# Kernel tuning notes

Measured on AMD Instinct MI355X. Metric: run time of the kernel, lower is better.

## Reference

```python
import jax, jax.numpy as jnp
import numpy as np

B, N, KNN, C, H, LK, CEMB, GDIM = 16, 512, 20, 256, 128, 4, 64, 64


def _lrelu(x, slope):
    return jnp.where(x >= 0, x, slope * x)


def _forward(img_feat, graph_feat, roi_mask_bit, prev_x_id, prev_y_id, knn_idx,
             conv_w, conv_b, pre_w1, pre_b1, pre_w2, pre_b2,
             g1_w, g1_gamma, g1_beta, g1_mean, g1_var,
             g2_w, g2_gamma, g2_beta, g2_mean, g2_var,
             q_w1, q_b1, q_w2, q_b2, q_w3, q_b3):
    lk = conv_w.shape[-1]
    bsz = img_feat.shape[0]
    # Index2Feat: conv with padding = lk-1 -> (B, CEMB, H+lk-1, W+lk-1)
    patches = jax.lax.conv_general_dilated(img_feat, conv_w, (1, 1), [(lk - 1, lk - 1)] * 2)
    patches = patches + conv_b[None, :, None, None]
    p = jnp.transpose(patches, (0, 2, 3, 1))  # (B, Hp, Wp, CEMB)
    bi = jnp.arange(bsz)[:, None]
    yy, xx = 2 * prev_y_id, 2 * prev_x_id
    sf1 = p[bi, yy, xx]
    sf2 = p[bi, yy + lk, xx]
    sf3 = p[bi, yy, xx + lk]
    sf4 = p[bi, yy + lk, xx + lk]
    local = jnp.concatenate([sf1, sf2, sf3, sf4], axis=-1)  # (B, N, 4*CEMB)
    local = local * jnp.transpose(roi_mask_bit, (0, 2, 1))  # detached mask
    local = jnp.concatenate([local, jnp.transpose(graph_feat, (0, 2, 1))], axis=-1)  # (B,N,320)
    # pre_graph MLP (LeakyReLU 0.01, doLastAct=True)
    h = _lrelu(local @ pre_w1 + pre_b1, 0.01)
    h = _lrelu(h @ pre_w2 + pre_b2, 0.01)  # (B, N, C)
    knn = knn_idx[0]  # (N, K) shared across batch

    def edgeconv(x, w, gamma, beta, mean, var):
        xk = x[:, knn]  # (B, N, K, C) neighbor gather
        xc = jnp.broadcast_to(x[:, :, None, :], xk.shape)
        e = jnp.concatenate([xk - xc, xc], axis=-1)  # (B, N, K, 2C)
        y = jnp.einsum('bnkc,oc->bnko', e, w)  # 1x1 conv, no bias
        y = (y - mean) * (gamma / jnp.sqrt(var + 1e-5)) + beta  # BN (inference)
        return _lrelu(y, 0.2).max(axis=2)  # max over k neighbors

    h = edgeconv(h, g1_w, g1_gamma, g1_beta, g1_mean, g1_var)
    h = edgeconv(h, g2_w, g2_gamma, g2_beta, g2_mean, g2_var)
    # query MLP (256 -> 256 -> 64 -> 2), LeakyReLU 0.01, no last act
    q = _lrelu(h @ q_w1 + q_b1, 0.01)
    q = _lrelu(q @ q_w2 + q_b2, 0.01)
    bits = q @ q_w3 + q_b3  # (B, N, 2)
    return jnp.transpose(bits, (0, 2, 1)), jnp.transpose(h, (0, 2, 1))


def setup_inputs() -> dict:
    key = jax.random.key(0)
    ks = jax.random.split(key, 24)
    s = 0.02
    img_feat = jax.random.normal(ks[0], (B, C, H, H), jnp.float32)
    graph_feat = jax.random.normal(ks[1], (B, GDIM, N), jnp.float32)
    roi_mask_bit = jnp.ones((B, 1, N), jnp.float32)
    prev_x_id = jax.random.randint(ks[2], (B, N), 0, H // 2, jnp.int32)
    prev_y_id = jax.random.randint(ks[3], (B, N), 0, H // 2, jnp.int32)
    # knn graph from normalized 3D keypoints (computed once at init in torch)
    p3d = jax.random.uniform(ks[4], (1, 3, N), jnp.float32, -1.0, 1.0)
    inner = -2.0 * jnp.einsum('bdn,bdm->bnm', p3d, p3d)
    xsq = jnp.sum(p3d ** 2, axis=1, keepdims=True)  # (1,1,N)
    pd = -xsq - inner - jnp.transpose(xsq, (0, 2, 1))
    knn_idx = jax.lax.top_k(pd, KNN)[1].astype(jnp.int32)  # (1, N, KNN)
    return {
        'img_feat': img_feat, 'graph_feat': graph_feat, 'roi_mask_bit': roi_mask_bit,
        'prev_x_id': prev_x_id, 'prev_y_id': prev_y_id, 'knn_idx': knn_idx,
        'conv_w': jax.random.normal(ks[5], (CEMB, C, LK, LK), jnp.float32) * s,
        'conv_b': jnp.zeros((CEMB,), jnp.float32),
        'pre_w1': jax.random.normal(ks[6], (4 * CEMB + GDIM, C), jnp.float32) * s,
        'pre_b1': jnp.zeros((C,), jnp.float32),
        'pre_w2': jax.random.normal(ks[7], (C, C), jnp.float32) * s,
        'pre_b2': jnp.zeros((C,), jnp.float32),
        'g1_w': jax.random.normal(ks[8], (C, 2 * C), jnp.float32) * s,
        'g1_gamma': jnp.ones((C,), jnp.float32), 'g1_beta': jnp.zeros((C,), jnp.float32),
        'g1_mean': jnp.zeros((C,), jnp.float32), 'g1_var': jnp.ones((C,), jnp.float32),
        'g2_w': jax.random.normal(ks[9], (C, 2 * C), jnp.float32) * s,
        'g2_gamma': jnp.ones((C,), jnp.float32), 'g2_beta': jnp.zeros((C,), jnp.float32),
        'g2_mean': jnp.zeros((C,), jnp.float32), 'g2_var': jnp.ones((C,), jnp.float32),
        'q_w1': jax.random.normal(ks[10], (C, C), jnp.float32) * s,
        'q_b1': jnp.zeros((C,), jnp.float32),
        'q_w2': jax.random.normal(ks[11], (C, 64), jnp.float32) * s,
        'q_b2': jnp.zeros((64,), jnp.float32),
        'q_w3': jax.random.normal(ks[12], (64, 2), jnp.float32) * s,
        'q_b3': jnp.zeros((2,), jnp.float32),
    }


def reference(img_feat, graph_feat, roi_mask_bit, prev_x_id, prev_y_id, knn_idx,
              conv_w, conv_b, pre_w1, pre_b1, pre_w2, pre_b2,
              g1_w, g1_gamma, g1_beta, g1_mean, g1_var,
              g2_w, g2_gamma, g2_beta, g2_mean, g2_var,
              q_w1, q_b1, q_w2, q_b2, q_w3, q_b3):
    return _forward(img_feat, graph_feat, roi_mask_bit, prev_x_id, prev_y_id, knn_idx,
                    conv_w, conv_b, pre_w1, pre_b1, pre_w2, pre_b2,
                    g1_w, g1_gamma, g1_beta, g1_mean, g1_var,
                    g2_w, g2_gamma, g2_beta, g2_mean, g2_var,
                    q_w1, q_b1, q_w2, q_b2, q_w3, q_b3)
```

## Files before the change

kernel.cpp:

```cpp
#include <hip/hip_runtime.h>


typedef __bf16 bf16_t;
typedef bf16_t bf16x8 __attribute__((ext_vector_type(8)));
typedef float  f32x4  __attribute__((ext_vector_type(4)));

static constexpr int BATCH = 16;
static constexpr int NPT   = 512;
static constexpr int PTS   = BATCH * NPT;
static constexpr int CONVM = PTS * 4;
static constexpr int CONVK = 4096;

static constexpr size_t OFF_WCONV_OLD = 0;
static constexpr size_t OFF_WCONVP    = OFF_WCONV_OLD + (size_t)64*4096*2;
static constexpr size_t OFF_WPRE1     = OFF_WCONVP    + (size_t)64*4096*2;
static constexpr size_t OFF_WPRE2     = OFF_WPRE1     + (size_t)256*320*2;
static constexpr size_t OFF_WEC1      = OFF_WPRE2     + (size_t)256*256*2;
static constexpr size_t OFF_WEC2      = OFF_WEC1      + (size_t)512*256*2;
static constexpr size_t OFF_WQ1       = OFF_WEC2      + (size_t)512*256*2;
static constexpr size_t OFF_WQ2       = OFF_WQ1       + (size_t)256*256*2;
static constexpr size_t OFF_LOCAL     = OFF_WQ2       + (size_t)64*256*2;
static constexpr size_t OFF_X         = OFF_LOCAL + (size_t)PTS*320*2;
static constexpr size_t OFF_Y         = OFF_X     + (size_t)PTS*256*2;
static constexpr size_t OFF_Z         = OFF_Y     + (size_t)PTS*256*2;
static constexpr size_t OFF_UNION     = OFF_Z     + (size_t)PTS*64*2;
static constexpr size_t AB_BYTES      = (size_t)PTS*512*4;
static constexpr size_t IMGT_BYTES    = (size_t)16*128*128*256*2;
static constexpr size_t WS_BASE       = OFF_UNION + AB_BYTES;
static constexpr size_t WS_FULL       = OFF_UNION + IMGT_BYTES;

static constexpr int WP_CONV  = 64*4096;
static constexpr int WP_CONVP = 64*4096;
static constexpr int WP_PRE1 = 256*320;
static constexpr int WP_PRE2 = 256*256;
static constexpr int WP_EC   = 512*256;
static constexpr int WP_Q1   = 256*256;
static constexpr int WP_Q2   = 64*256;
static constexpr int WP_TOTAL = WP_CONV + WP_CONVP + WP_PRE1 + WP_PRE2 + 2*WP_EC + WP_Q1 + WP_Q2;

__global__ __launch_bounds__(256) void wprep_kernel(
    const float* __restrict__ conv_w, const float* __restrict__ pre_w1,
    const float* __restrict__ pre_w2, const float* __restrict__ g1_w,
    const float* __restrict__ g2_w,   const float* __restrict__ q_w1,
    const float* __restrict__ q_w2,
    bf16_t* __restrict__ wt_conv, bf16_t* __restrict__ wt_convp,
    bf16_t* __restrict__ wt_pre1,
    bf16_t* __restrict__ wt_pre2, bf16_t* __restrict__ wt_ec1,
    bf16_t* __restrict__ wt_ec2,  bf16_t* __restrict__ wt_q1,
    bf16_t* __restrict__ wt_q2)
{
    int i = blockIdx.x * 256 + threadIdx.x;
    if (i >= WP_TOTAL) return;
    if (i < WP_CONV) { wt_conv[i] = (bf16_t)conv_w[i]; return; }
    i -= WP_CONV;
    if (i < WP_CONVP) {
        const int o = i >> 12, pix = (i >> 8) & 15, c = i & 255;
        wt_convp[i] = (bf16_t)conv_w[((o * 256 + c) << 4) + pix]; return; }
    i -= WP_CONVP;
    if (i < WP_PRE1) { int n = i / 320, k = i - n * 320;
        wt_pre1[i] = (bf16_t)pre_w1[k * 256 + n]; return; }
    i -= WP_PRE1;
    if (i < WP_PRE2) { int n = i >> 8, k = i & 255;
        wt_pre2[i] = (bf16_t)pre_w2[k * 256 + n]; return; }
    i -= WP_PRE2;
    if (i < WP_EC) { int n = i >> 8, k = i & 255;
        wt_ec1[i] = (bf16_t)(n < 256 ? g1_w[n * 512 + k] : g1_w[(n - 256) * 512 + 256 + k]);
        return; }
    i -= WP_EC;
    if (i < WP_EC) { int n = i >> 8, k = i & 255;
        wt_ec2[i] = (bf16_t)(n < 256 ? g2_w[n * 512 + k] : g2_w[(n - 256) * 512 + 256 + k]);
        return; }
    i -= WP_EC;
    if (i < WP_Q1) { int n = i >> 8, k = i & 255;
        wt_q1[i] = (bf16_t)q_w1[k * 256 + n]; return; }
    i -= WP_Q1;
    { int n = i >> 8, k = i & 255;
        wt_q2[i] = (bf16_t)q_w2[k * 64 + n]; }
}

__global__ __launch_bounds__(256) void transpose_img(
    const float* __restrict__ img, bf16_t* __restrict__ imgT)
{
    __shared__ float T[64][65];
    const int bid = blockIdx.x;
    const int cc = bid & 3;
    const int xh = (bid >> 2) & 1;
    const int y  = (bid >> 3) & 127;
    const int b  = bid >> 10;
    const int t = threadIdx.x;
    const int x0 = xh * 64, c0 = cc * 64;
    {
        const int px = t & 63, cr = t >> 6;
        const float* src = img + ((size_t)(b * 256 + c0 + cr) * 128 + y) * 128 + x0 + px;
        #pragma unroll
        for (int i = 0; i < 16; ++i)
            T[cr + i * 4][px] = src[(size_t)i * 4 * 16384];
    }
    __syncthreads();
    {
        const int cl = t & 63, pr = t >> 6;
        bf16_t* dst = imgT + ((size_t)(b * 128 + y) * 128 + x0) * 256 + c0 + cl;
        #pragma unroll
        for (int i = 0; i < 16; ++i) {
            const int pxl = pr + i * 4;
            dst[(size_t)pxl * 256] = (bf16_t)T[cl][pxl];
        }
    }
}

__global__ __launch_bounds__(256) void conv_gather_gemm2(
    const bf16_t* __restrict__ imgT,
    const bf16_t* __restrict__ Wc,
    const float* __restrict__ conv_b, const float* __restrict__ roi,
    const int* __restrict__ px, const int* __restrict__ py,
    bf16_t* __restrict__ local)
{
    __shared__ bf16_t As[64][136];
    __shared__ bf16_t Bs[64][136];
    const int tid = threadIdx.x, lane = tid & 63, wave = tid >> 6;
    const int wm = wave & 1, wn = wave >> 1;
    const int row0 = blockIdx.x * 64;
    const int sm = tid >> 2, sq = tid & 3;
    const int r = row0 + sm, corner = r & 3, pnt = r >> 2, b = pnt >> 9;
    const int oy = 2 * py[pnt] + (corner & 1) * 4;
    const int ox = 2 * px[pnt] + ((corner >> 1) & 1) * 4;
    const bf16_t* imgb = imgT + (size_t)b * (128 * 128 * 256);
    const int e0 = sq * 8;

    f32x4 acc[2][2] = {};
    #pragma unroll 1
    for (int s = 0; s < 32; ++s) {
        const int pix = s >> 1, h = s & 1;
        const int iy = oy - 3 + (pix >> 2), ix = ox - 3 + (pix & 3);
        if (((unsigned)iy < 128u) && ((unsigned)ix < 128u)) {
            const bf16_t* srcA = imgb + ((size_t)(iy * 128 + ix)) * 256 + h * 128 + e0;
            #pragma unroll
            for (int i = 0; i < 4; ++i)
                *(uint4*)&As[sm][e0 + i * 32] = *(const uint4*)(srcA + i * 32);
        } else {
            const uint4 z = {0, 0, 0, 0};
            #pragma unroll
            for (int i = 0; i < 4; ++i)
                *(uint4*)&As[sm][e0 + i * 32] = z;
        }
        {
            const bf16_t* srcB = Wc + (size_t)sm * 4096 + pix * 256 + h * 128 + e0;
            #pragma unroll
            for (int i = 0; i < 4; ++i)
                *(uint4*)&Bs[sm][e0 + i * 32] = *(const uint4*)(srcB + i * 32);
        }
        __syncthreads();
        #pragma unroll
        for (int kk = 0; kk < 128; kk += 32) {
            const int kf = kk + ((lane >> 4) << 3);
            bf16x8 a0 = *(const bf16x8*)&As[wm * 32 + (lane & 15)][kf];
            bf16x8 a1 = *(const bf16x8*)&As[wm * 32 + 16 + (lane & 15)][kf];
            bf16x8 b0 = *(const bf16x8*)&Bs[wn * 32 + (lane & 15)][kf];
            bf16x8 b1 = *(const bf16x8*)&Bs[wn * 32 + 16 + (lane & 15)][kf];
            acc[0][0] = __builtin_amdgcn_mfma_f32_16x16x32_bf16(a0, b0, acc[0][0], 0, 0, 0);
            acc[0][1] = __builtin_amdgcn_mfma_f32_16x16x32_bf16(a0, b1, acc[0][1], 0, 0, 0);
            acc[1][0] = __builtin_amdgcn_mfma_f32_16x16x32_bf16(a1, b0, acc[1][0], 0, 0, 0);
            acc[1][1] = __builtin_amdgcn_mfma_f32_16x16x32_bf16(a1, b1, acc[1][1], 0, 0, 0);
        }
        __syncthreads();
    }
    const int crow = (lane >> 4) << 2;
    const int ccol = lane & 15;
    #pragma unroll
    for (int i = 0; i < 2; ++i) {
        #pragma unroll
        for (int j = 0; j < 2; ++j) {
            const int o = wn * 32 + j * 16 + ccol;
            const float bv = conv_b[o];
            #pragma unroll
            for (int rg = 0; rg < 4; ++rg) {
                const int gr = row0 + wm * 32 + i * 16 + crow + rg;
                const int cn = gr & 3;
                const int pp = gr >> 2;
                const float v = (acc[i][j][rg] + bv) * roi[pp];
                local[(size_t)pp * 320 + cn * 64 + o] = (bf16_t)v;
            }
        }
    }
}

__global__ __launch_bounds__(256) void conv_gather_gemm(
    const float* __restrict__ img, const bf16_t* __restrict__ Wc,
    const float* __restrict__ conv_b, const float* __restrict__ roi,
    const int* __restrict__ px, const int* __restrict__ py,
    bf16_t* __restrict__ local)
{
    __shared__ bf16_t As[64][72];
    __shared__ bf16_t Bs[64][72];
    const int tid = threadIdx.x;
    const int lane = tid & 63;
    const int wave = tid >> 6;
    const int wm = wave & 1, wn = wave >> 1;
    const int row0 = blockIdx.x * 64;
    const int sm = tid >> 2;
    const int cq = tid & 3;
    const int r = row0 + sm;
    const int corner = r & 3;
    const int pnt = r >> 2;
    const int b = pnt >> 9;
    const int oy = 2 * py[pnt] + (corner & 1) * 4;
    const int ox = 2 * px[pnt] + ((corner >> 1) & 1) * 4;
    const int iy0 = oy - 3, ix0 = ox - 3;
    const float* imgb = img + (size_t)b * (256 * 128 * 128);

    f32x4 acc[2][2] = {};
    for (int kt = 0; kt < CONVK; kt += 64) {
        {
            const int c = (kt >> 4) + cq;
            const float* ip = imgb + (size_t)c * (128 * 128);
            alignas(16) bf16_t vals[16];
            #pragma unroll
            for (int ky = 0; ky < 4; ++ky) {
                const int iy = iy0 + ky;
                const bool yok = (unsigned)iy < 128u;
                #pragma unroll
                for (int kx = 0; kx < 4; ++kx) {
                    const int ix = ix0 + kx;
                    float v = (yok && (unsigned)ix < 128u) ? ip[iy * 128 + ix] : 0.0f;
                    vals[ky * 4 + kx] = (bf16_t)v;
                }
            }
            *(uint4*)&As[sm][cq * 16]     = *(const uint4*)&vals[0];
            *(uint4*)&As[sm][cq * 16 + 8] = *(const uint4*)&vals[8];
        }
        {
            const bf16_t* src = Wc + (size_t)sm * CONVK + kt + cq * 16;
            *(uint4*)&Bs[sm][cq * 16]     = *(const uint4*)src;
            *(uint4*)&Bs[sm][cq * 16 + 8] = *(const uint4*)(src + 8);
        }
        __syncthreads();
        #pragma unroll
        for (int kk = 0; kk < 64; kk += 32) {
            const int kf = kk + ((lane >> 4) << 3);
            bf16x8 a0 = *(const bf16x8*)&As[wm * 32 + (lane & 15)][kf];
            bf16x8 a1 = *(const bf16x8*)&As[wm * 32 + 16 + (lane & 15)][kf];
            bf16x8 b0 = *(const bf16x8*)&Bs[wn * 32 + (lane & 15)][kf];
            bf16x8 b1 = *(const bf16x8*)&Bs[wn * 32 + 16 + (lane & 15)][kf];
            acc[0][0] = __builtin_amdgcn_mfma_f32_16x16x32_bf16(a0, b0, acc[0][0], 0, 0, 0);
            acc[0][1] = __builtin_amdgcn_mfma_f32_16x16x32_bf16(a0, b1, acc[0][1], 0, 0, 0);
            acc[1][0] = __builtin_amdgcn_mfma_f32_16x16x32_bf16(a1, b0, acc[1][0], 0, 0, 0);
            acc[1][1] = __builtin_amdgcn_mfma_f32_16x16x32_bf16(a1, b1, acc[1][1], 0, 0, 0);
        }
        __syncthreads();
    }
    const int crow = (lane >> 4) << 2;
    const int ccol = lane & 15;
    #pragma unroll
    for (int i = 0; i < 2; ++i) {
        #pragma unroll
        for (int j = 0; j < 2; ++j) {
            const int o = wn * 32 + j * 16 + ccol;
            const float bv = conv_b[o];
            #pragma unroll
            for (int rg = 0; rg < 4; ++rg) {
                const int gr = row0 + wm * 32 + i * 16 + crow + rg;
                const int cn = gr & 3;
                const int pp = gr >> 2;
                const float v = (acc[i][j][rg] + bv) * roi[pp];
                local[(size_t)pp * 320 + cn * 64 + o] = (bf16_t)v;
            }
        }
    }
}

__global__ __launch_bounds__(256) void graph_fill(
    const float* __restrict__ g, bf16_t* __restrict__ local)
{
    const int e = blockIdx.x * 256 + threadIdx.x;
    const int j = e & 63, p = e >> 6;
    const int b = p >> 9, n = p & 511;
    local[(size_t)p * 320 + 256 + j] = (bf16_t)g[((size_t)(b * 64 + j) << 9) + n];
}

template<int K, int N, int ACT>
__global__ __launch_bounds__(256) void gemm_bf16(
    const bf16_t* __restrict__ A, const bf16_t* __restrict__ Bt,
    const float* __restrict__ bias, float slope,
    bf16_t* __restrict__ outB, float* __restrict__ outF)
{
    __shared__ bf16_t As[64][72];
    __shared__ bf16_t Bs[64][72];
    const int tid = threadIdx.x;
    const int lane = tid & 63;
    const int wave = tid >> 6;
    const int wm = wave & 1, wn = wave >> 1;
    const int row0 = blockIdx.x * 64;
    const int col0 = blockIdx.y * 64;
    const int sm = tid >> 2;
    const int sq = (tid & 3) << 4;

    f32x4 acc[2][2] = {};
    for (int kt = 0; kt < K; kt += 64) {
        {
            const bf16_t* src = A + (size_t)(row0 + sm) * K + kt + sq;
            *(uint4*)&As[sm][sq]     = *(const uint4*)src;
            *(uint4*)&As[sm][sq + 8] = *(const uint4*)(src + 8);
        }
        {
            const bf16_t* src = Bt + (size_t)(col0 + sm) * K + kt + sq;
            *(uint4*)&Bs[sm][sq]     = *(const uint4*)src;
            *(uint4*)&Bs[sm][sq + 8] = *(const uint4*)(src + 8);
        }
        __syncthreads();
        #pragma unroll
        for (int kk = 0; kk < 64; kk += 32) {
            const int kf = kk + ((lane >> 4) << 3);
            bf16x8 a0 = *(const bf16x8*)&As[wm * 32 + (lane & 15)][kf];
            bf16x8 a1 = *(const bf16x8*)&As[wm * 32 + 16 + (lane & 15)][kf];
            bf16x8 b0 = *(const bf16x8*)&Bs[wn * 32 + (lane & 15)][kf];
            bf16x8 b1 = *(const bf16x8*)&Bs[wn * 32 + 16 + (lane & 15)][kf];
            acc[0][0] = __builtin_amdgcn_mfma_f32_16x16x32_bf16(a0, b0, acc[0][0], 0, 0, 0);
            acc[0][1] = __builtin_amdgcn_mfma_f32_16x16x32_bf16(a0, b1, acc[0][1], 0, 0, 0);
            acc[1][0] = __builtin_amdgcn_mfma_f32_16x16x32_bf16(a1, b0, acc[1][0], 0, 0, 0);
            acc[1][1] = __builtin_amdgcn_mfma_f32_16x16x32_bf16(a1, b1, acc[1][1], 0, 0, 0);
        }
        __syncthreads();
    }
    const int crow = (lane >> 4) << 2;
    const int ccol = lane & 15;
    #pragma unroll
    for (int i = 0; i < 2; ++i) {
        #pragma unroll
        for (int j = 0; j < 2; ++j) {
            const int gcol = col0 + wn * 32 + j * 16 + ccol;
            const float bv = bias ? bias[gcol] : 0.0f;
            #pragma unroll
            for (int rg = 0; rg < 4; ++rg) {
                const int grow = row0 + wm * 32 + i * 16 + crow + rg;
                float v = acc[i][j][rg] + bv;
                if (ACT == 1) v = v >= 0.0f ? v : slope * v;
                if (outB) outB[(size_t)grow * N + gcol] = (bf16_t)v;
                if (outF) outF[(size_t)grow * N + gcol] = v;
            }
        }
    }
}

__global__ __launch_bounds__(256) void edge_combine(
    const float* __restrict__ AB, const int* __restrict__ knn,
    const float* __restrict__ gamma, const float* __restrict__ beta,
    const float* __restrict__ mean,  const float* __restrict__ var,
    bf16_t* __restrict__ outB, float* __restrict__ outT)
{
    const int p = blockIdx.x;
    const int b = p >> 9, n = p & 511;
    const int o = threadIdx.x;
    const float sc = gamma[o] / sqrtf(var[o] + 1e-5f);
    const float sh = beta[o] - mean[o] * sc;
    const float* rowp = AB + (size_t)p * 512;
    const float d = rowp[256 + o] - rowp[o];
    const float* batch = AB + ((size_t)(b << 9)) * 512;
    float m = -3.4e38f;
    #pragma unroll 4
    for (int k = 0; k < 20; ++k) {
        const int q = knn[n * 20 + k];
        const float v = batch[(size_t)q * 512 + o] + d;
        float y = v * sc + sh;
        y = y >= 0.0f ? y : 0.2f * y;
        m = fmaxf(m, y);
    }
    outB[(size_t)p * 256 + o] = (bf16_t)m;
    if (outT) outT[((size_t)(b * 256 + o) << 9) + n] = m;
}

__global__ __launch_bounds__(256) void q3_kernel(
    const bf16_t* __restrict__ Z, const float* __restrict__ w3,
    const float* __restrict__ b3, float* __restrict__ out)
{
    const int p = blockIdx.x * 256 + threadIdx.x;
    const int b = p >> 9, n = p & 511;
    const bf16_t* q = Z + (size_t)p * 64;
    float s0 = b3[0], s1 = b3[1];
    #pragma unroll
    for (int c = 0; c < 64; ++c) {
        const float v = (float)q[c];
        s0 += v * w3[2 * c];
        s1 += v * w3[2 * c + 1];
    }
    out[(size_t)(b * 2 + 0) * 512 + n] = s0;
    out[(size_t)(b * 2 + 1) * 512 + n] = s1;
}

extern "C" void kernel_launch(void* const* d_in, const int* in_sizes, int n_in,
                              void* d_out, int out_size, void* d_ws, size_t ws_size,
                              hipStream_t stream)
{
    const float* img      = (const float*)d_in[0];
    const float* graph    = (const float*)d_in[1];
    const float* roi      = (const float*)d_in[2];
    const int*   px       = (const int*)d_in[3];
    const int*   py       = (const int*)d_in[4];
    const int*   knn      = (const int*)d_in[5];
    const float* conv_w   = (const float*)d_in[6];
    const float* conv_b   = (const float*)d_in[7];
    const float* pre_w1   = (const float*)d_in[8];
    const float* pre_b1   = (const float*)d_in[9];
    const float* pre_w2   = (const float*)d_in[10];
    const float* pre_b2   = (const float*)d_in[11];
    const float* g1_w     = (const float*)d_in[12];
    const float* g1_gamma = (const float*)d_in[13];
    const float* g1_beta  = (const float*)d_in[14];
    const float* g1_mean  = (const float*)d_in[15];
    const float* g1_var   = (const float*)d_in[16];
    const float* g2_w     = (const float*)d_in[17];
    const float* g2_gamma = (const float*)d_in[18];
    const float* g2_beta  = (const float*)d_in[19];
    const float* g2_mean  = (const float*)d_in[20];
    const float* g2_var   = (const float*)d_in[21];
    const float* q_w1     = (const float*)d_in[22];
    const float* q_b1     = (const float*)d_in[23];
    const float* q_w2     = (const float*)d_in[24];
    const float* q_b2     = (const float*)d_in[25];
    const float* q_w3     = (const float*)d_in[26];
    const float* q_b3     = (const float*)d_in[27];
    float* out = (float*)d_out;

    if (ws_size < WS_BASE) return;

    char* ws = (char*)d_ws;
    bf16_t* wt_conv  = (bf16_t*)(ws + OFF_WCONV_OLD);
    bf16_t* wt_convp = (bf16_t*)(ws + OFF_WCONVP);
    bf16_t* wt_pre1  = (bf16_t*)(ws + OFF_WPRE1);
    bf16_t* wt_pre2  = (bf16_t*)(ws + OFF_WPRE2);
    bf16_t* wt_ec1   = (bf16_t*)(ws + OFF_WEC1);
    bf16_t* wt_ec2   = (bf16_t*)(ws + OFF_WEC2);
    bf16_t* wt_q1    = (bf16_t*)(ws + OFF_WQ1);
    bf16_t* wt_q2    = (bf16_t*)(ws + OFF_WQ2);
    bf16_t* local    = (bf16_t*)(ws + OFF_LOCAL);
    bf16_t* X        = (bf16_t*)(ws + OFF_X);
    bf16_t* Y        = (bf16_t*)(ws + OFF_Y);
    bf16_t* Z        = (bf16_t*)(ws + OFF_Z);
    float*  AB       = (float*)(ws + OFF_UNION);
    bf16_t* imgT     = (bf16_t*)(ws + OFF_UNION);

    const bool big = ws_size >= WS_FULL;

    wprep_kernel<<<(WP_TOTAL + 255) / 256, 256, 0, stream>>>(
        conv_w, pre_w1, pre_w2, g1_w, g2_w, q_w1, q_w2,
        wt_conv, wt_convp, wt_pre1, wt_pre2, wt_ec1, wt_ec2, wt_q1, wt_q2);

    if (big) {
        transpose_img<<<16 * 128 * 2 * 4, 256, 0, stream>>>(img, imgT);
        conv_gather_gemm2<<<CONVM / 64, 256, 0, stream>>>(
            imgT, wt_convp, conv_b, roi, px, py, local);
    } else {
        conv_gather_gemm<<<CONVM / 64, 256, 0, stream>>>(
            img, wt_conv, conv_b, roi, px, py, local);
    }

    graph_fill<<<(PTS * 64) / 256, 256, 0, stream>>>(graph, local);

    gemm_bf16<320, 256, 1><<<dim3(PTS / 64, 4), 256, 0, stream>>>(
        local, wt_pre1, pre_b1, 0.01f, X, nullptr);
    gemm_bf16<256, 256, 1><<<dim3(PTS / 64, 4), 256, 0, stream>>>(
        X, wt_pre2, pre_b2, 0.01f, Y, nullptr);

    gemm_bf16<256, 512, 0><<<dim3(PTS / 64, 8), 256, 0, stream>>>(
        Y, wt_ec1, nullptr, 0.0f, nullptr, AB);
    edge_combine<<<PTS, 256, 0, stream>>>(
        AB, knn, g1_gamma, g1_beta, g1_mean, g1_var, X, nullptr);

    gemm_bf16<256, 512, 0><<<dim3(PTS / 64, 8), 256, 0, stream>>>(
        X, wt_ec2, nullptr, 0.0f, nullptr, AB);
    edge_combine<<<PTS, 256, 0, stream>>>(
        AB, knn, g2_gamma, g2_beta, g2_mean, g2_var, Y, out + 16384);

    gemm_bf16<256, 256, 1><<<dim3(PTS / 64, 4), 256, 0, stream>>>(
        Y, wt_q1, q_b1, 0.01f, X, nullptr);
    gemm_bf16<256, 64, 1><<<dim3(PTS / 64, 1), 256, 0, stream>>>(
        X, wt_q2, q_b2, 0.01f, Z, nullptr);
    q3_kernel<<<PTS / 256, 256, 0, stream>>>(Z, q_w3, q_b3, out);
}
```

Before: 268.2 us.

## Pad transposed image with zero border and shrink conv gather tile to 32 rows

The transposed bf16 image is now stored with a 4-pixel zero border (136x136), filled by a new pad kernel, so the conv gather no longer needs per-pixel bounds checks or zero-fill branches. The transpose now writes packed bf16 pairs instead of single elements. The conv gather GEMM uses 32-row M tiles, doubling the block count, with each wave computing one A fragment against two B fragments. In exchange there is an extra kernel launch, a larger workspace requirement, and more total B-weight loads across blocks.

```diff
diff --git a/kernel.cpp b/kernel.cpp
--- a/kernel.cpp
+++ b/kernel.cpp
@@ -2,6 +2,7 @@
 
 
 typedef __bf16 bf16_t;
+typedef bf16_t bf16x2 __attribute__((ext_vector_type(2)));
 typedef bf16_t bf16x8 __attribute__((ext_vector_type(8)));
 typedef float  f32x4  __attribute__((ext_vector_type(4)));
 
@@ -10,6 +11,9 @@
 static constexpr int PTS   = BATCH * NPT;
 static constexpr int CONVM = PTS * 4;
 static constexpr int CONVK = 4096;
+
+static constexpr int PY_DIM = 136;
+static constexpr size_t IMG_BSTRIDE = (size_t)PY_DIM * PY_DIM * 256;
 
 static constexpr size_t OFF_WCONV_OLD = 0;
 static constexpr size_t OFF_WCONVP    = OFF_WCONV_OLD + (size_t)64*4096*2;
@@ -25,7 +29,7 @@
 static constexpr size_t OFF_Z         = OFF_Y     + (size_t)PTS*256*2;
 static constexpr size_t OFF_UNION     = OFF_Z     + (size_t)PTS*64*2;
 static constexpr size_t AB_BYTES      = (size_t)PTS*512*4;
-static constexpr size_t IMGT_BYTES    = (size_t)16*128*128*256*2;
+static constexpr size_t IMGT_BYTES    = (size_t)16*IMG_BSTRIDE*2;
 static constexpr size_t WS_BASE       = OFF_UNION + AB_BYTES;
 static constexpr size_t WS_FULL       = OFF_UNION + IMGT_BYTES;
 
@@ -78,6 +82,23 @@
         wt_q2[i] = (bf16_t)q_w2[k * 64 + n]; }
 }
 
+static constexpr int PAD_THREADS = 16 * 2112 * 32;
+
+__global__ __launch_bounds__(256) void pad_border(bf16_t* __restrict__ imgT)
+{
+    const int idx = blockIdx.x * 256 + threadIdx.x;
+    if (idx >= PAD_THREADS) return;
+    const int t = idx & 31;
+    int pi = idx >> 5;
+    const int b = pi / 2112; pi -= b * 2112;
+    int y, x;
+    if (pi < 544)      { y = pi / 136;              x = pi % 136; }
+    else if (pi < 1088){ int j = pi - 544; y = 132 + j / 136; x = j % 136; }
+    else { int j = pi - 1088; y = 4 + (j >> 3); int k = j & 7; x = (k < 4) ? k : (128 + k); }
+    const uint4 z = {0, 0, 0, 0};
+    ((uint4*)(imgT + ((size_t)(b * PY_DIM + y) * PY_DIM + x) * 256))[t] = z;
+}
+
 __global__ __launch_bounds__(256) void transpose_img(
     const float* __restrict__ img, bf16_t* __restrict__ imgT)
 {
@@ -98,88 +119,81 @@
     }
     __syncthreads();
     {
-        const int cl = t & 63, pr = t >> 6;
-        bf16_t* dst = imgT + ((size_t)(b * 128 + y) * 128 + x0) * 256 + c0 + cl;
-        #pragma unroll
-        for (int i = 0; i < 16; ++i) {
-            const int pxl = pr + i * 4;
-            dst[(size_t)pxl * 256] = (bf16_t)T[cl][pxl];
-        }
-    }
-}
-
-__global__ __launch_bounds__(256) void conv_gather_gemm2(
+        const int cl2 = (t & 31) * 2, pr = t >> 5;
+        bf16_t* dst = imgT + ((size_t)(b * PY_DIM + y + 4) * PY_DIM + x0 + 4) * 256 + c0 + cl2;
+        #pragma unroll
+        for (int i = 0; i < 8; ++i) {
+            const int pxl = pr + i * 8;
+            bf16x2 w;
+            w[0] = (bf16_t)T[cl2][pxl];
+            w[1] = (bf16_t)T[cl2 + 1][pxl];
+            *(bf16x2*)(dst + (size_t)pxl * 256) = w;
+        }
+    }
+}
+
+__global__ __launch_bounds__(256) void conv_gather_gemm3(
     const bf16_t* __restrict__ imgT,
     const bf16_t* __restrict__ Wc,
     const float* __restrict__ conv_b, const float* __restrict__ roi,
     const int* __restrict__ px, const int* __restrict__ py,
     bf16_t* __restrict__ local)
 {
-    __shared__ bf16_t As[64][136];
+    __shared__ bf16_t As[32][136];
     __shared__ bf16_t Bs[64][136];
     const int tid = threadIdx.x, lane = tid & 63, wave = tid >> 6;
     const int wm = wave & 1, wn = wave >> 1;
-    const int row0 = blockIdx.x * 64;
-    const int sm = tid >> 2, sq = tid & 3;
-    const int r = row0 + sm, corner = r & 3, pnt = r >> 2, b = pnt >> 9;
-    const int oy = 2 * py[pnt] + (corner & 1) * 4;
-    const int ox = 2 * px[pnt] + ((corner >> 1) & 1) * 4;
-    const bf16_t* imgb = imgT + (size_t)b * (128 * 128 * 256);
-    const int e0 = sq * 8;
-
-    f32x4 acc[2][2] = {};
+    const int row0 = blockIdx.x * 32;
+
+    const int ra = tid >> 3, seg = tid & 7;
+    const int r = row0 + ra, corner = r & 3, pnt = r >> 2, b = pnt >> 9;
+    const int oy = 2 * py[pnt] + (corner & 1) * 4 + 1;
+    const int ox = 2 * px[pnt] + ((corner >> 1) & 1) * 4 + 1;
+    const bf16_t* imgb = imgT + (size_t)b * IMG_BSTRIDE;
+    const int rb = tid >> 2, sq = tid & 3;
+    const bf16_t* wrow = Wc + (size_t)rb * 4096 + sq * 8;
+
+    f32x4 acc[2] = {};
     #pragma unroll 1
     for (int s = 0; s < 32; ++s) {
         const int pix = s >> 1, h = s & 1;
-        const int iy = oy - 3 + (pix >> 2), ix = ox - 3 + (pix & 3);
-        if (((unsigned)iy < 128u) && ((unsigned)ix < 128u)) {
-            const bf16_t* srcA = imgb + ((size_t)(iy * 128 + ix)) * 256 + h * 128 + e0;
+        const int iy = oy + (pix >> 2), ix = ox + (pix & 3);
+        {
+            const bf16_t* srcA = imgb + ((size_t)(iy * PY_DIM + ix)) * 256 + h * 128 + seg * 16;
+            *(uint4*)&As[ra][seg * 16]     = *(const uint4*)srcA;
+            *(uint4*)&As[ra][seg * 16 + 8] = *(const uint4*)(srcA + 8);
+        }
+        {
+            const bf16_t* srcB = wrow + pix * 256 + h * 128;
             #pragma unroll
             for (int i = 0; i < 4; ++i)
-                *(uint4*)&As[sm][e0 + i * 32] = *(const uint4*)(srcA + i * 32);
-        } else {
-            const uint4 z = {0, 0, 0, 0};
-            #pragma unroll
-            for (int i = 0; i < 4; ++i)
-                *(uint4*)&As[sm][e0 + i * 32] = z;
-        }
-        {
-            const bf16_t* srcB = Wc + (size_t)sm * 4096 + pix * 256 + h * 128 + e0;
-            #pragma unroll
-            for (int i = 0; i < 4; ++i)
-                *(uint4*)&Bs[sm][e0 + i * 32] = *(const uint4*)(srcB + i * 32);
+                *(uint4*)&Bs[rb][sq * 8 + i * 32] = *(const uint4*)(srcB + i * 32);
         }
         __syncthreads();
         #pragma unroll
         for (int kk = 0; kk < 128; kk += 32) {
             const int kf = kk + ((lane >> 4) << 3);
-            bf16x8 a0 = *(const bf16x8*)&As[wm * 32 + (lane & 15)][kf];
-            bf16x8 a1 = *(const bf16x8*)&As[wm * 32 + 16 + (lane & 15)][kf];
+            bf16x8 a  = *(const bf16x8*)&As[wm * 16 + (lane & 15)][kf];
             bf16x8 b0 = *(const bf16x8*)&Bs[wn * 32 + (lane & 15)][kf];
             bf16x8 b1 = *(const bf16x8*)&Bs[wn * 32 + 16 + (lane & 15)][kf];
-            acc[0][0] = __builtin_amdgcn_mfma_f32_16x16x32_bf16(a0, b0, acc[0][0], 0, 0, 0);
-            acc[0][1] = __builtin_amdgcn_mfma_f32_16x16x32_bf16(a0, b1, acc[0][1], 0, 0, 0);
-            acc[1][0] = __builtin_amdgcn_mfma_f32_16x16x32_bf16(a1, b0, acc[1][0], 0, 0, 0);
-            acc[1][1] = __builtin_amdgcn_mfma_f32_16x16x32_bf16(a1, b1, acc[1][1], 0, 0, 0);
+            acc[0] = __builtin_amdgcn_mfma_f32_16x16x32_bf16(a, b0, acc[0], 0, 0, 0);
+            acc[1] = __builtin_amdgcn_mfma_f32_16x16x32_bf16(a, b1, acc[1], 0, 0, 0);
         }
         __syncthreads();
     }
     const int crow = (lane >> 4) << 2;
     const int ccol = lane & 15;
     #pragma unroll
-    for (int i = 0; i < 2; ++i) {
-        #pragma unroll
-        for (int j = 0; j < 2; ++j) {
-            const int o = wn * 32 + j * 16 + ccol;
-            const float bv = conv_b[o];
-            #pragma unroll
-            for (int rg = 0; rg < 4; ++rg) {
-                const int gr = row0 + wm * 32 + i * 16 + crow + rg;
-                const int cn = gr & 3;
-                const int pp = gr >> 2;
-                const float v = (acc[i][j][rg] + bv) * roi[pp];
-                local[(size_t)pp * 320 + cn * 64 + o] = (bf16_t)v;
-            }
+    for (int j = 0; j < 2; ++j) {
+        const int o = wn * 32 + j * 16 + ccol;
+        const float bv = conv_b[o];
+        #pragma unroll
+        for (int rg = 0; rg < 4; ++rg) {
+            const int gr = row0 + wm * 16 + crow + rg;
+            const int cn = gr & 3;
+            const int pp = gr >> 2;
+            const float v = (acc[j][rg] + bv) * roi[pp];
+            local[(size_t)pp * 320 + cn * 64 + o] = (bf16_t)v;
         }
     }
 }
@@ -445,8 +459,9 @@
         wt_conv, wt_convp, wt_pre1, wt_pre2, wt_ec1, wt_ec2, wt_q1, wt_q2);
 
     if (big) {
+        pad_border<<<(PAD_THREADS + 255) / 256, 256, 0, stream>>>(imgT);
         transpose_img<<<16 * 128 * 2 * 4, 256, 0, stream>>>(img, imgT);
-        conv_gather_gemm2<<<CONVM / 64, 256, 0, stream>>>(
+        conv_gather_gemm3<<<CONVM / 32, 256, 0, stream>>>(
             imgT, wt_convp, conv_b, roi, px, py, local);
     } else {
         conv_gather_gemm<<<CONVM / 64, 256, 0, stream>>>(
```

Measured after the change: 265.5 us. Within noise of the previous version (-1.0%).
